# Kernel tuning notes

Measured on AMD Instinct MI355X. Metric: run time of the kernel, lower is better.

## Reference

```python
import jax, jax.numpy as jnp
import numpy as np

# HyenaConfig constants (match init_kwargs)
SEQ_LEN = 8192
HIDDEN_DIM = 768
EMB_DIM = 3
FILTER_ORDER = 64
FAST_DECAY_PCT = 0.3
SLOW_DECAY_PCT = 1.5
TARGET = 0.01
SHIFT = 0.0


def setup_inputs() -> dict:
    key = jax.random.key(0)
    ks = jax.random.split(key, 9)
    return {
        "x": jax.random.normal(ks[0], (8, SEQ_LEN, HIDDEN_DIM), dtype=jnp.float32),
        "w_in": jax.random.normal(ks[1], (EMB_DIM, FILTER_ORDER), dtype=jnp.float32),
        "b_in": jax.random.normal(ks[2], (FILTER_ORDER,), dtype=jnp.float32),
        "freq_in": jnp.ones((1, FILTER_ORDER), dtype=jnp.float32),
        "w_h0": jax.random.normal(ks[3], (FILTER_ORDER, FILTER_ORDER), dtype=jnp.float32),
        "b_h0": jax.random.normal(ks[4], (FILTER_ORDER,), dtype=jnp.float32),
        "freq_h0": jnp.ones((1, FILTER_ORDER), dtype=jnp.float32),
        "w_h1": jax.random.normal(ks[5], (FILTER_ORDER, FILTER_ORDER), dtype=jnp.float32),
        "b_h1": jax.random.normal(ks[6], (FILTER_ORDER,), dtype=jnp.float32),
        "freq_h1": jnp.ones((1, FILTER_ORDER), dtype=jnp.float32),
        "w_out": jax.random.normal(ks[7], (FILTER_ORDER, HIDDEN_DIM), dtype=jnp.float32),
        "bias": jax.random.normal(ks[8], (HIDDEN_DIM,), dtype=jnp.float32),
        "L": SEQ_LEN,
    }


def _pos_emb(L):
    # PositionalEmbedding.init: t in [0,1], z = [t, Re(e^{-i f w}), Im(e^{-i f w})]
    t = jnp.linspace(0.0, 1.0, L, dtype=jnp.float32).reshape(L, 1)
    bands = (EMB_DIM - 1) // 2
    t_rescaled = jnp.linspace(0.0, L - 1, L, dtype=jnp.float32).reshape(L, 1)
    w = 2.0 * jnp.pi * t_rescaled / L  # (L, 1)
    f = jnp.linspace(1e-4, bands - 1, bands, dtype=jnp.float32).reshape(1, bands)
    phase = f * w  # (L, bands)
    z = jnp.concatenate([t, jnp.cos(phase), -jnp.sin(phase)], axis=-1)  # (L, EMB_DIM)
    return z, t


def _filter_k(L, w_in, b_in, freq_in, w_h0, b_h0, freq_h0, w_h1, b_h1, freq_h1, w_out):
    z, t = _pos_emb(L)
    # ImplicitFilterMLP: Linear -> Sin -> (Linear -> Sin) x2 -> Linear (no bias)
    h = jnp.sin(freq_in * (z @ w_in + b_in))
    h = jnp.sin(freq_h0 * (h @ w_h0 + b_h0))
    h = jnp.sin(freq_h1 * (h @ w_h1 + b_h1))
    h = h @ w_out  # (L, HIDDEN_DIM)
    # ExponentialModulation
    max_decay = jnp.log(TARGET) / FAST_DECAY_PCT
    min_decay = jnp.log(TARGET) / SLOW_DECAY_PCT
    deltas = jnp.linspace(min_decay, max_decay, HIDDEN_DIM, dtype=jnp.float32)  # (D,)
    decay = jnp.exp(-t * jnp.abs(deltas))  # (L, D)
    return h * (decay + SHIFT)


def _fft_conv(u, k, bias):
    # u: (B, L, D), k: (L, D)
    seqlen = u.shape[-2]
    fft_size = 2 * seqlen
    u_f = jnp.fft.rfft(u, n=fft_size, axis=-2)
    k_f = jnp.fft.rfft(k[None], n=fft_size, axis=-2) / fft_size
    y = jnp.fft.irfft(u_f * k_f, n=fft_size, axis=-2)[..., :seqlen, :]
    return y + bias.reshape(1, 1, -1)


def reference(x, w_in, b_in, freq_in, w_h0, b_h0, freq_h0, w_h1, b_h1, freq_h1,
              w_out, bias, L):
    k = _filter_k(L, w_in, b_in, freq_in, w_h0, b_h0, freq_h0, w_h1, b_h1,
                  freq_h1, w_out)  # (L, D)
    return _fft_conv(x, k, bias)
```

## Files before the change

kernel.cpp:

```cpp
#include <hip/hip_runtime.h>
#include <stdint.h>

typedef __bf16   bf16x8 __attribute__((ext_vector_type(8)));
typedef float    f32x4  __attribute__((ext_vector_type(4)));
typedef uint32_t u32x4  __attribute__((ext_vector_type(4)));
typedef uint32_t u32x2  __attribute__((ext_vector_type(2)));
typedef unsigned short u16x8 __attribute__((ext_vector_type(8)));

#define L_SEQ 8192
#define DIM   768
#define DROW  8768


__global__ __launch_bounds__(256) void pad_kernel(uint32_t* __restrict__ dupG)
{
  int d = blockIdx.x;
  const int NPAD = 31 + (DROW - 8224);
  for (int j = threadIdx.x; j < NPAD; j += 256) {
    int i = (j < 31) ? j : 8224 + (j - 31);
    dupG[(size_t)d * DROW + i] = 0u;
  }
}

__global__ __launch_bounds__(256) void filter_kernel(
    const float* __restrict__ w_in, const float* __restrict__ b_in,
    const float* __restrict__ freq_in,
    const float* __restrict__ w_h0, const float* __restrict__ b_h0,
    const float* __restrict__ freq_h0,
    const float* __restrict__ w_h1, const float* __restrict__ b_h1,
    const float* __restrict__ freq_h1,
    const float* __restrict__ w_out,
    uint32_t* __restrict__ dupG)
{
  __shared__ float h1[33][65];
  __shared__ float h2[33][65];
  __shared__ unsigned short kv[33][64];
  __shared__ float wch[64][64];

  const int c = blockIdx.x;
  const int sbase = c << 5;
  const int tid = threadIdx.x;

  for (int p = tid; p < 33 * 64; p += 256) {
    int j = p >> 6, n = p & 63;
    int s = sbase - 1 + j;
    float t  = s * (1.0f / 8191.0f);
    float ph = s * (float)(6.283185307179586 * 1e-4 / 8192.0);
    float a = t * w_in[n] + cosf(ph) * w_in[64 + n] + (-sinf(ph)) * w_in[128 + n] + b_in[n];
    h1[j][n] = sinf(freq_in[n] * a);
  }
  for (int p = tid; p < 64 * 64; p += 256) wch[p >> 6][p & 63] = w_h0[p];
  __syncthreads();
  for (int p = tid; p < 33 * 64; p += 256) {
    int j = p >> 6, n = p & 63;
    float a = b_h0[n];
    for (int r = 0; r < 64; ++r) a += h1[j][r] * wch[r][n];
    h2[j][n] = sinf(freq_h0[n] * a);
  }
  __syncthreads();
  for (int p = tid; p < 64 * 64; p += 256) wch[p >> 6][p & 63] = w_h1[p];
  __syncthreads();
  for (int p = tid; p < 33 * 64; p += 256) {
    int j = p >> 6, n = p & 63;
    float a = b_h1[n];
    for (int r = 0; r < 64; ++r) a += h2[j][r] * wch[r][n];
    h1[j][n] = sinf(freq_h1[n] * a);
  }
  __syncthreads();

  for (int dc = 0; dc < 12; ++dc) {
    for (int p = tid; p < 64 * 64; p += 256) {
      int r = p >> 6, dd = p & 63;
      wch[r][dd] = w_out[r * DIM + dc * 64 + dd];
    }
    __syncthreads();
    for (int p = tid; p < 33 * 64; p += 256) {
      int j = p >> 6, dd = p & 63;
      float a = 0.0f;
      for (int r = 0; r < 64; ++r) a += h1[j][r] * wch[r][dd];
      int s = sbase - 1 + j;
      int d = dc * 64 + dd;
      float delta = fabsf(-3.070113457f - 12.280453827f * (d * (1.0f / 767.0f)));
      float t = s * (1.0f / 8191.0f);
      float val = (s < 0) ? 0.0f : a * expf(-t * delta) * 6.103515625e-05f;
      kv[j][dd] = __builtin_bit_cast(unsigned short, (__bf16)val);
    }
    __syncthreads();
    for (int p = tid; p < 32 * 64; p += 256) {
      int j = p >> 6, dd = p & 63;
      int d = dc * 64 + dd;
      int i = 8223 - (sbase + j);
      dupG[(size_t)d * DROW + i] =
          (uint32_t)kv[j + 1][dd] | ((uint32_t)kv[j][dd] << 16);
    }
    if (c == 255 && tid < 64) {
      int d = dc * 64 + tid;
      dupG[(size_t)d * DROW + 31] = ((uint32_t)kv[32][tid] << 16);
    }
    __syncthreads();
  }
}

__global__ __launch_bounds__(256) void transpose_in_kernel(
    const float* __restrict__ x, unsigned short* __restrict__ uT)
{
  __shared__ unsigned short tile[64][68];
  int b = blockIdx.z;
  int t0 = blockIdx.y * 64;
  int d0 = blockIdx.x * 64;
  int tid = threadIdx.x;

  int ld = tid & 15;
  int tq = tid >> 4;
#pragma unroll
  for (int it = 0; it < 4; ++it) {
    int trow = tq + 16 * it;
    f32x4 xv = *(const f32x4*)&x[((size_t)b * L_SEQ + t0 + trow) * DIM + d0 + 4 * ld];
    unsigned short s0 = __builtin_bit_cast(unsigned short, (__bf16)xv[0]);
    unsigned short s1 = __builtin_bit_cast(unsigned short, (__bf16)xv[1]);
    unsigned short s2 = __builtin_bit_cast(unsigned short, (__bf16)xv[2]);
    unsigned short s3 = __builtin_bit_cast(unsigned short, (__bf16)xv[3]);
    u32x2 pk = { (uint32_t)s0 | ((uint32_t)s1 << 16),
                 (uint32_t)s2 | ((uint32_t)s3 << 16) };
    *(u32x2*)&tile[trow][4 * ld] = pk;
  }
  __syncthreads();

  int l = tid & 63, w = tid >> 6;
  int toct = l & 7;
#pragma unroll
  for (int it = 0; it < 2; ++it) {
    int d = 8 * w + 32 * it + (l >> 3);
    u16x8 o;
#pragma unroll
    for (int c2 = 0; c2 < 8; ++c2) o[c2] = tile[8 * toct + c2][d];
    *(u16x8*)&uT[((size_t)(d0 + d) * 8 + b) * L_SEQ + t0 + 8 * toct] = o;
  }
}

#define LOADFRAG(dst, absdw) {                                    \
    int _p = ((absdw) & 2047);                                    \
    u32x4 _u = { buf[_p], buf[_p + 2], buf[_p + 4], buf[_p + 6] };\
    dst = __builtin_bit_cast(bf16x8, _u); }

__global__ __launch_bounds__(256) void conv_kernel(
    const uint32_t* __restrict__ dupG,
    const unsigned short* __restrict__ uT,
    unsigned short* __restrict__ yT)
{
  const int d   = blockIdx.y;
  const int T0  = blockIdx.x << 10;
  const int tid = threadIdx.x;
  const int lane = tid & 63;
  const int w    = tid >> 6;
  const int m = lane & 15, q = lane >> 4;
  const int h = (lane >> 3) & 1;
  __shared__ uint32_t buf[2080];

  f32x4 acc[8] = {};
  bf16x8 fr2[8];
  bf16x8 pa[8];
  bf16x8 zfr = {};

  float delta = fabsf(-3.070113457f - 12.280453827f * (d * (1.0f / 767.0f)));
  int S = (int)(8191.0f * 3.5065578f / delta);
  int tau_start = T0 - S;
  tau_start = (tau_start < 0) ? 0 : (tau_start & ~31);
  int niter = ((T0 + 992 - tau_start) >> 5) + 1;
  niter = (niter + 7) & ~7;

  const uint32_t* dG = dupG + (size_t)d * DROW;
  const unsigned short* uTd = uT + ((size_t)d << 16);

  int i0 = 7200 + tau_start - T0;

  int a_off = ((lane & 7) << 14) + ((tau_start - 16 + (h << 4) + (q << 3)) << 1);

#pragma unroll
  for (int rr = 0; rr < 8; ++rr)
    pa[rr] = *(const bf16x8*)((const char*)uTd + a_off + (rr << 6));

  for (int j4 = tid * 4; j4 < 1280; j4 += 1024) {
    int i = i0 + j4;
    u32x4 v = *(const u32x4*)&dG[i];
    int pos = i & 2047;
    *(u32x4*)&buf[pos] = v;
    if (pos < 32) *(u32x4*)&buf[2048 + pos] = v;
  }
  __syncthreads();

  const bool kill = (tau_start == 0) & (h == 0) & (q < 2);
  if (kill) pa[0] = zfr;

  int vb = i0 + 1007 - (w << 8) - m + (q << 3);
  int chunk_i = i0 + 1280;

  LOADFRAG(fr2[7], vb - 32);
  LOADFRAG(fr2[6], vb - 64);
  LOADFRAG(fr2[5], vb - 96);
  LOADFRAG(fr2[4], vb - 128);
  LOADFRAG(fr2[3], vb - 160);
  LOADFRAG(fr2[2], vb - 192);
  LOADFRAG(fr2[1], vb - 224);

#define MFMA_J(rr, j)                                                          \
  acc[j] = __builtin_amdgcn_mfma_f32_16x16x32_bf16(                            \
      afrag, fr2[((rr) - (j)) & 7], acc[j], 0, 0, 0);

#define BODY(rr) {                                                             \
    LOADFRAG(fr2[(rr) & 7], vb + ((rr) << 5));                                 \
    bf16x8 afrag = pa[rr];                                                     \
    pa[rr] = *(const bf16x8*)((const char*)uTd + a_off + ((rr) << 6) + 512);   \
    MFMA_J(rr, 1) MFMA_J(rr, 2) MFMA_J(rr, 3) MFMA_J(rr, 4)                    \
    MFMA_J(rr, 5) MFMA_J(rr, 6) MFMA_J(rr, 7) MFMA_J(rr, 0)                    \
  }

  for (int nn = 0; nn < niter; nn += 8) {
    u32x4 stage = {};
    int si4 = chunk_i + (tid << 2);
    if (tid < 64) {
      int iv = (si4 < 8740) ? si4 : 8740;
      stage = *(const u32x4*)&dG[iv];
    }
    BODY(0) BODY(1) BODY(2) BODY(3)
    BODY(4) BODY(5) BODY(6) BODY(7)
    if (tid < 64) {
      int pos = si4 & 2047;
      *(u32x4*)&buf[pos] = stage;
      if (pos < 32) *(u32x4*)&buf[2048 + pos] = stage;
    }
    __syncthreads();
    a_off += 512; vb += 256; chunk_i += 256;
  }

#pragma unroll
  for (int j = 0; j < 8; ++j) {
    int tb_ = T0 + (w << 8) + (j << 5) + m;
#pragma unroll
    for (int r = 0; r < 4; ++r) {
      int row = q * 4 + r;
      int bb = row & 7;
      int hh = row >> 3;
      yT[((size_t)(d * 8 + bb) << 13) + tb_ + (hh << 4)] =
          __builtin_bit_cast(unsigned short, (__bf16)acc[j][r]);
    }
  }
}

__global__ __launch_bounds__(256) void transpose_out_kernel(
    const unsigned short* __restrict__ yT, const float* __restrict__ bias,
    float* __restrict__ out)
{
  __shared__ unsigned short tile[64][68];
  int b = blockIdx.z;
  int t0 = blockIdx.y * 64;
  int d0 = blockIdx.x * 64;
  int tid = threadIdx.x;

  int l = tid & 63, w = tid >> 6;
  int toct = l & 7;
#pragma unroll
  for (int it = 0; it < 2; ++it) {
    int d = 8 * w + 32 * it + (l >> 3);
    u16x8 o = *(const u16x8*)&yT[((size_t)(d0 + d) * 8 + b) * L_SEQ + t0 + 8 * toct];
#pragma unroll
    for (int c2 = 0; c2 < 8; ++c2) tile[8 * toct + c2][d] = o[c2];
  }
  __syncthreads();

  int ld = tid & 15;
  int tq = tid >> 4;
  f32x4 bs = *(const f32x4*)&bias[d0 + 4 * ld];
#pragma unroll
  for (int it = 0; it < 4; ++it) {
    int trow = tq + 16 * it;
    u32x2 pk = *(const u32x2*)&tile[trow][4 * ld];
    f32x4 ov;
    ov[0] = (float)__builtin_bit_cast(__bf16, (unsigned short)(pk[0] & 0xffff)) + bs[0];
    ov[1] = (float)__builtin_bit_cast(__bf16, (unsigned short)(pk[0] >> 16))    + bs[1];
    ov[2] = (float)__builtin_bit_cast(__bf16, (unsigned short)(pk[1] & 0xffff)) + bs[2];
    ov[3] = (float)__builtin_bit_cast(__bf16, (unsigned short)(pk[1] >> 16))    + bs[3];
    *(f32x4*)&out[((size_t)b * L_SEQ + t0 + trow) * DIM + d0 + 4 * ld] = ov;
  }
}

extern "C" void kernel_launch(void* const* d_in, const int* in_sizes, int n_in,
                              void* d_out, int out_size, void* d_ws, size_t ws_size,
                              hipStream_t stream)
{
  const float* x       = (const float*)d_in[0];
  const float* w_in    = (const float*)d_in[1];
  const float* b_in    = (const float*)d_in[2];
  const float* freq_in = (const float*)d_in[3];
  const float* w_h0    = (const float*)d_in[4];
  const float* b_h0    = (const float*)d_in[5];
  const float* freq_h0 = (const float*)d_in[6];
  const float* w_h1    = (const float*)d_in[7];
  const float* b_h1    = (const float*)d_in[8];
  const float* freq_h1 = (const float*)d_in[9];
  const float* w_out   = (const float*)d_in[10];
  const float* bias    = (const float*)d_in[11];

  char* ws = (char*)d_ws;
  uint32_t* dupG = (uint32_t*)(ws);
  unsigned short* uT = (unsigned short*)(ws + 26935296);
  unsigned short* yT = (unsigned short*)(ws + 127598592);
  float* out = (float*)d_out;

  hipLaunchKernelGGL(pad_kernel, dim3(DIM), dim3(256), 0, stream, dupG);
  hipLaunchKernelGGL(filter_kernel, dim3(256), dim3(256), 0, stream,
                     w_in, b_in, freq_in, w_h0, b_h0, freq_h0,
                     w_h1, b_h1, freq_h1, w_out, dupG);
  hipLaunchKernelGGL(transpose_in_kernel, dim3(12, 128, 8), dim3(256), 0, stream, x, uT);
  hipLaunchKernelGGL(conv_kernel, dim3(8, DIM), dim3(256), 0, stream, dupG, uT, yT);
  hipLaunchKernelGGL(transpose_out_kernel, dim3(12, 128, 8), dim3(256), 0, stream,
                     yT, bias, out);
}
```

Measured before the change: 941.7 us.

## Stage conv A operands through LDS via async global_load_lds double buffering

The conv kernel stops loading the eight A fragments per iteration straight from global memory into registers. It now copies each 8-step chunk of the input slab into a double-buffered LDS tile with global_load_lds, overlapping that copy with the MFMA work, and reads fragments from LDS using a padded stride. The filter kernel is also split across 4 blocks in y so the w_out projection runs with more parallelism, at the cost of recomputing the MLP layers 4 times. The change lowers register pressure and global latency in the hot loop but adds LDS traffic and relies on correct sync ordering with the existing barrier.

```diff
diff --git a/kernel.cpp b/kernel.cpp
--- a/kernel.cpp
+++ b/kernel.cpp
@@ -38,6 +38,7 @@
   __shared__ float wch[64][64];
 
   const int c = blockIdx.x;
+  const int dcg = blockIdx.y;
   const int sbase = c << 5;
   const int tid = threadIdx.x;
 
@@ -68,7 +69,7 @@
   }
   __syncthreads();
 
-  for (int dc = 0; dc < 12; ++dc) {
+  for (int dc = dcg * 3; dc < dcg * 3 + 3; ++dc) {
     for (int p = tid; p < 64 * 64; p += 256) {
       int r = p >> 6, dd = p & 63;
       wch[r][dd] = w_out[r * DIM + dc * 64 + dd];
@@ -143,6 +144,11 @@
     u32x4 _u = { buf[_p], buf[_p + 2], buf[_p + 4], buf[_p + 6] };\
     dst = __builtin_bit_cast(bf16x8, _u); }
 
+#define DSREAD_A(rr, P) (*(const bf16x8*)((P) + abyte + ((rr) << 6)))
+
+typedef __attribute__((address_space(1))) const void g_void;
+typedef __attribute__((address_space(3))) void lds_void;
+
 __global__ __launch_bounds__(256) void conv_kernel(
     const uint32_t* __restrict__ dupG,
     const unsigned short* __restrict__ uT,
@@ -156,10 +162,11 @@
   const int m = lane & 15, q = lane >> 4;
   const int h = (lane >> 3) & 1;
   __shared__ uint32_t buf[2080];
+  __shared__ __align__(16) char As0[5120];
+  __shared__ __align__(16) char As1[5120];
 
   f32x4 acc[8] = {};
   bf16x8 fr2[8];
-  bf16x8 pa[8];
   bf16x8 zfr = {};
 
   float delta = fabsf(-3.070113457f - 12.280453827f * (d * (1.0f / 767.0f)));
@@ -174,11 +181,20 @@
 
   int i0 = 7200 + tau_start - T0;
 
-  int a_off = ((lane & 7) << 14) + ((tau_start - 16 + (h << 4) + (q << 3)) << 1);
-
-#pragma unroll
-  for (int rr = 0; rr < 8; ++rr)
-    pa[rr] = *(const bf16x8*)((const char*)uTd + a_off + (rr << 6));
+  int s0 = tid;
+  int b0 = s0 / 34, r0 = s0 - 34 * b0;
+  const char* ga0 = (const char*)uTd + b0 * 16384 + (tau_start - 16 + r0 * 8) * 2;
+  int s1 = 256 + lane;
+  int b1 = s1 / 34, r1 = s1 - 34 * b1;
+  const char* ga1 = (const char*)uTd + b1 * 16384 + (tau_start - 16 + r1 * 8) * 2;
+
+  const char* Acur = As0;
+  const char* Anxt = As1;
+
+  __builtin_amdgcn_global_load_lds((g_void*)ga0, (lds_void*)(As0 + (w << 10)), 16, 0, 0);
+  if (w == 0)
+    __builtin_amdgcn_global_load_lds((g_void*)ga1, (lds_void*)(As0 + 4096), 16, 0, 0);
+  ga0 += 512; ga1 += 512;
 
   for (int j4 = tid * 4; j4 < 1280; j4 += 1024) {
     int i = i0 + j4;
@@ -189,8 +205,7 @@
   }
   __syncthreads();
 
-  const bool kill = (tau_start == 0) & (h == 0) & (q < 2);
-  if (kill) pa[0] = zfr;
+  const int abyte = 544 * (lane & 7) + (h << 5) + (q << 4);
 
   int vb = i0 + 1007 - (w << 8) - m + (q << 3);
   int chunk_i = i0 + 1280;
@@ -203,34 +218,49 @@
   LOADFRAG(fr2[2], vb - 192);
   LOADFRAG(fr2[1], vb - 224);
 
+  bf16x8 pa_c = DSREAD_A(0, Acur);
+  if ((tau_start == 0) & (h == 0) & (q < 2)) pa_c = zfr;
+
 #define MFMA_J(rr, j)                                                          \
   acc[j] = __builtin_amdgcn_mfma_f32_16x16x32_bf16(                            \
       afrag, fr2[((rr) - (j)) & 7], acc[j], 0, 0, 0);
 
-#define BODY(rr) {                                                             \
+#define BODYP(rr) {                                                            \
     LOADFRAG(fr2[(rr) & 7], vb + ((rr) << 5));                                 \
-    bf16x8 afrag = pa[rr];                                                     \
-    pa[rr] = *(const bf16x8*)((const char*)uTd + a_off + ((rr) << 6) + 512);   \
+    bf16x8 afrag = pa_c;                                                       \
+    pa_c = DSREAD_A((rr) + 1, Acur);                                           \
     MFMA_J(rr, 1) MFMA_J(rr, 2) MFMA_J(rr, 3) MFMA_J(rr, 4)                    \
     MFMA_J(rr, 5) MFMA_J(rr, 6) MFMA_J(rr, 7) MFMA_J(rr, 0)                    \
   }
+#define BODYL(rr) {                                                            \
+    LOADFRAG(fr2[(rr) & 7], vb + ((rr) << 5));                                 \
+    bf16x8 afrag = pa_c;                                                       \
+    MFMA_J(rr, 1) MFMA_J(rr, 2) MFMA_J(rr, 3) MFMA_J(rr, 4)                    \
+    MFMA_J(rr, 5) MFMA_J(rr, 6) MFMA_J(rr, 7) MFMA_J(rr, 0)                    \
+  }
 
   for (int nn = 0; nn < niter; nn += 8) {
+    __builtin_amdgcn_global_load_lds((g_void*)ga0, (lds_void*)(Anxt + (w << 10)), 16, 0, 0);
+    if (w == 0)
+      __builtin_amdgcn_global_load_lds((g_void*)ga1, (lds_void*)(Anxt + 4096), 16, 0, 0);
+    ga0 += 512; ga1 += 512;
     u32x4 stage = {};
     int si4 = chunk_i + (tid << 2);
     if (tid < 64) {
       int iv = (si4 < 8740) ? si4 : 8740;
       stage = *(const u32x4*)&dG[iv];
     }
-    BODY(0) BODY(1) BODY(2) BODY(3)
-    BODY(4) BODY(5) BODY(6) BODY(7)
+    BODYP(0) BODYP(1) BODYP(2) BODYP(3)
+    BODYP(4) BODYP(5) BODYP(6) BODYL(7)
     if (tid < 64) {
       int pos = si4 & 2047;
       *(u32x4*)&buf[pos] = stage;
       if (pos < 32) *(u32x4*)&buf[2048 + pos] = stage;
     }
     __syncthreads();
-    a_off += 512; vb += 256; chunk_i += 256;
+    { const char* t_ = Acur; Acur = Anxt; Anxt = t_; }
+    vb += 256; chunk_i += 256;
+    pa_c = DSREAD_A(0, Acur);
   }
 
 #pragma unroll
@@ -308,7 +338,7 @@
   float* out = (float*)d_out;
 
   hipLaunchKernelGGL(pad_kernel, dim3(DIM), dim3(256), 0, stream, dupG);
-  hipLaunchKernelGGL(filter_kernel, dim3(256), dim3(256), 0, stream,
+  hipLaunchKernelGGL(filter_kernel, dim3(256, 4), dim3(256), 0, stream,
                      w_in, b_in, freq_in, w_h0, b_h0, freq_h0,
                      w_h1, b_h1, freq_h1, w_out, dupG);
   hipLaunchKernelGGL(transpose_in_kernel, dim3(12, 128, 8), dim3(256), 0, stream, x, uT);
```

Result: faster. 760.8 us (-19.2%).
